# Performance work log

Measured on AMD Instinct MI355X. Metric: run time of the kernel, lower is better.

## Reference

```python
import jax, jax.numpy as jnp
import numpy as np

N_NODES = 50000
N_EDGES = 800000
D = 64
N_LAYERS = 3  # zip(convs(4), batchnorms(3)) truncates to 3 executed layers
N_GRAPHS = 32
EPS_BN = 1e-5
NEG_SLOPE = 0.2


def segment_softmax(logits, seg, n):
    m = jax.ops.segment_max(logits, seg, num_segments=n)
    m = jnp.where(jnp.isfinite(m), m, 0.0)
    z = jnp.exp(logits - m[seg])
    s = jax.ops.segment_sum(z, seg, num_segments=n)
    return z / (s[seg] + 1e-16)


def setup_inputs() -> dict:
    key = jax.random.key(0)
    ks = jax.random.split(key, 16)
    s = 0.1
    return {
        "x": jax.random.normal(ks[0], (N_NODES, D), jnp.float32),
        "edge_index": jax.random.randint(ks[1], (2, N_EDGES), 0, N_NODES),
        "edge_attr": jax.random.normal(ks[2], (N_EDGES, D), jnp.float32),
        "batch": jnp.sort(jax.random.randint(ks[3], (N_NODES,), 0, N_GRAPHS)),
        # EdgeConvLayer MLP params (stacked over layers)
        "em_w1": jax.random.normal(ks[4], (N_LAYERS, 3 * D, D)) * s,
        "em_b1": jnp.zeros((N_LAYERS, D)),
        "em_w2": jax.random.normal(ks[5], (N_LAYERS, D, D)) * s,
        "em_b2": jnp.zeros((N_LAYERS, D)),
        # GATConv params (heads=1, add_self_loops=False)
        "gat_w": jax.random.normal(ks[6], (N_LAYERS, D, D)) * s,
        "att_src": jax.random.normal(ks[7], (N_LAYERS, D)) * s,
        "att_dst": jax.random.normal(ks[8], (N_LAYERS, D)) * s,
        "edge_w": jax.random.normal(ks[9], (N_LAYERS, D, D)) * s,
        "att_edge": jax.random.normal(ks[10], (N_LAYERS, D)) * s,
        "gat_bias": jnp.zeros((N_LAYERS, D)),
        # BatchNorm params
        "bn_gamma": jnp.ones((N_LAYERS, D)),
        "bn_beta": jnp.zeros((N_LAYERS, D)),
        # readout MLP
        "mlp_w1": jax.random.normal(ks[11], (D, D)) * s,
        "mlp_b1": jnp.zeros((D,)),
        "mlp_w2": jax.random.normal(ks[12], (D, D // 2)) * s,
        "mlp_b2": jnp.zeros((D // 2,)),
        "mlp_w3": jax.random.normal(ks[13], (D // 2, 1)) * s,
        "mlp_b3": jnp.zeros((1,)),
    }


def reference(x, edge_index, edge_attr, batch, em_w1, em_b1, em_w2, em_b2,
              gat_w, att_src, att_dst, edge_w, att_edge, gat_bias,
              bn_gamma, bn_beta, mlp_w1, mlp_b1, mlp_w2, mlp_b2, mlp_w3, mlp_b3):
    row, col = edge_index[0], edge_index[1]
    n = x.shape[0]
    for l in range(N_LAYERS):
        # MetaLayer edge model: cat(src, dst, edge_attr) -> 2-layer MLP
        cat = jnp.concatenate([x[row], x[col], edge_attr], axis=1)  # (E, 3D)
        eh = jax.nn.relu(cat @ em_w1[l] + em_b1[l])
        edge_attr = eh @ em_w2[l] + em_b2[l]  # (E, D)
        # GATConv, heads=1: shared linear for src/dst
        xw = x @ gat_w[l]  # (N, D)
        a_edge = edge_attr @ (edge_w[l] @ att_edge[l])  # fused lin_edge + att_edge dot
        logits = (xw @ att_src[l])[row] + (xw @ att_dst[l])[col] + a_edge
        alpha = segment_softmax(jax.nn.leaky_relu(logits, NEG_SLOPE), col, n)
        h = jax.ops.segment_sum(alpha[:, None] * xw[row], col, num_segments=n) + gat_bias[l]
        # BatchNorm (training batch stats) + ReLU
        mu = h.mean(axis=0)
        var = h.var(axis=0)
        x = jax.nn.relu((h - mu) * jax.lax.rsqrt(var + EPS_BN) * bn_gamma[l] + bn_beta[l])
    # global mean pool over graphs
    sums = jax.ops.segment_sum(x, batch, num_segments=N_GRAPHS)
    cnt = jax.ops.segment_sum(jnp.ones((n,), x.dtype), batch, num_segments=N_GRAPHS)
    g = sums / jnp.maximum(cnt, 1.0)[:, None]
    h = jax.nn.relu(g @ mlp_w1 + mlp_b1)
    h = jax.nn.relu(h @ mlp_w2 + mlp_b2)
    return h @ mlp_w3 + mlp_b3  # (N_GRAPHS, 1)
```

## Files before the change

### kernel.cpp

```cpp
#include <hip/hip_runtime.h>


#define NN 50000
#define NE 800000
#define DP 68
#define NEG_SLOPE 0.2f

typedef __attribute__((ext_vector_type(8))) __bf16 bf16x8;
typedef __attribute__((ext_vector_type(4))) float f32x4;

__device__ __forceinline__ float4 ld4(const float* __restrict__ p){ return *(const float4* __restrict__)p; }
__device__ __forceinline__ void st4(float* __restrict__ p, float4 v){ *(float4* __restrict__)p = v; }
__device__ __forceinline__ float4 f4zero(){ return make_float4(0.f,0.f,0.f,0.f); }
__device__ __forceinline__ float4 f4add(float4 a, float4 b){
  return make_float4(a.x+b.x, a.y+b.y, a.z+b.z, a.w+b.w);
}
__device__ __forceinline__ float4 f4fma(float a, float4 b, float4 c){
  return make_float4(fmaf(a,b.x,c.x), fmaf(a,b.y,c.y), fmaf(a,b.z,c.z), fmaf(a,b.w,c.w));
}
__device__ __forceinline__ float f4dot(float4 a, float4 b){
  return fmaf(a.x,b.x, fmaf(a.y,b.y, fmaf(a.z,b.z, a.w*b.w)));
}
__device__ __forceinline__ bf16x8 cvt8(float4 a, float4 b){
  bf16x8 r;
  r[0]=(__bf16)a.x; r[1]=(__bf16)a.y; r[2]=(__bf16)a.z; r[3]=(__bf16)a.w;
  r[4]=(__bf16)b.x; r[5]=(__bf16)b.y; r[6]=(__bf16)b.z; r[7]=(__bf16)b.w;
  return r;
}
__device__ __forceinline__ bf16x8 addpack8(bf16x8 a, bf16x8 b){
  bf16x8 r;
#pragma unroll
  for (int e = 0; e < 8; ++e) r[e] = (__bf16)((float)a[e] + (float)b[e]);
  return r;
}
__device__ __forceinline__ ushort4 pack4(float4 v){
  ushort4 u;
  u.x = __builtin_bit_cast(unsigned short, (__bf16)v.x);
  u.y = __builtin_bit_cast(unsigned short, (__bf16)v.y);
  u.z = __builtin_bit_cast(unsigned short, (__bf16)v.z);
  u.w = __builtin_bit_cast(unsigned short, (__bf16)v.w);
  return u;
}
__device__ __forceinline__ float4 bnrelu4(float4 v, const float* sc, const float* sh, int d){
  return make_float4(
    fmaxf(fmaf(v.x, sc[d+0], sh[d+0]), 0.f),
    fmaxf(fmaf(v.y, sc[d+1], sh[d+1]), 0.f),
    fmaxf(fmaf(v.z, sc[d+2], sh[d+2]), 0.f),
    fmaxf(fmaf(v.w, sc[d+3], sh[d+3]), 0.f));
}

__device__ __forceinline__ void gemm_tile(const float* inT, const float* W,
                                          int el0, int d0, float4 acc[4]){
#pragma unroll 4
  for (int kc = 0; kc < 16; ++kc){
    float4 w0 = ld4(&W[(kc*4+0)*64 + d0]);
    float4 w1 = ld4(&W[(kc*4+1)*64 + d0]);
    float4 w2 = ld4(&W[(kc*4+2)*64 + d0]);
    float4 w3 = ld4(&W[(kc*4+3)*64 + d0]);
#pragma unroll
    for (int i = 0; i < 4; ++i){
      float4 iv = ld4(&inT[(el0+i)*DP + kc*4]);
      acc[i] = f4fma(iv.x, w0, acc[i]);
      acc[i] = f4fma(iv.y, w1, acc[i]);
      acc[i] = f4fma(iv.z, w2, acc[i]);
      acc[i] = f4fma(iv.w, w3, acc[i]);
    }
  }
}

__global__ __launch_bounds__(256) void hist_kernel(const int* __restrict__ ei_col,
                                                   int* __restrict__ cnt){
  int e = blockIdx.x * 256 + threadIdx.x;
  atomicAdd(&cnt[ei_col[e]], 1);
}

__global__ __launch_bounds__(256) void scan_kernel(const int* __restrict__ cnt,
                                                   int* __restrict__ off){
  __shared__ int wsum[4];
  __shared__ int carry_s;
  const int t = threadIdx.x;
  const int lane = t & 63, w = t >> 6;
  if (t == 0) carry_s = 0;
  __syncthreads();
  for (int base = 0; base < NN; base += 256){
    int idx = base + t;
    int v = (idx < NN) ? cnt[idx] : 0;
    int x = v;
#pragma unroll
    for (int o = 1; o < 64; o <<= 1){
      int u = __shfl_up(x, o);
      if (lane >= o) x += u;
    }
    if (lane == 63) wsum[w] = x;
    __syncthreads();
    int wo = carry_s;
#pragma unroll
    for (int k = 0; k < 4; ++k) if (k < w) wo += wsum[k];
    int incl = x + wo;
    if (idx < NN) off[idx] = incl - v;
    __syncthreads();
    if (t == 255) carry_s = incl;
    __syncthreads();
  }
  if (t == 0) off[NN] = carry_s;
}

__global__ __launch_bounds__(256) void scatter_kernel(
    const int* __restrict__ ei, const int* __restrict__ off, int* __restrict__ cur,
    int* __restrict__ srow, int* __restrict__ scol, int* __restrict__ perm){
  int e = blockIdx.x * 256 + threadIdx.x;
  int r = ei[e], c = ei[NE + e];
  int pos = off[c] + atomicAdd(&cur[c], 1);
  srow[pos] = r; scol[pos] = c; perm[pos] = e;
}

__global__ __launch_bounds__(256) void graph_bounds(const int* __restrict__ batch,
                                                    int* __restrict__ goff){
  int n = blockIdx.x * 256 + threadIdx.x;
  if (n >= NN) return;
  int bn = batch[n];
  int bp = (n == 0) ? -1 : batch[n-1];
  for (int g = bp + 1; g <= bn; ++g) goff[g] = n;
  if (n == NN - 1){ for (int g = bn + 1; g <= 32; ++g) goff[g] = NN; }
}

__global__ __launch_bounds__(256) void prep_weights(
    const float* __restrict__ em_w1, const float* __restrict__ em_w2,
    const float* __restrict__ edge_w, const float* __restrict__ att_edge,
    __bf16* __restrict__ w1f, __bf16* __restrict__ w2f, float* __restrict__ vbuf)
{
  const int l = blockIdx.x, t = threadIdx.x;
  const float* W1 = em_w1 + l*12288 + 8192;
  const float* W2 = em_w2 + l*4096;
  for (int p = t; p < 512; p += 256){
    int li = p & 63, ks = (p >> 6) & 1, nt = p >> 7;
    int kbase = ks*32 + (li >> 4)*8;
    int j = nt*16 + (li & 15);
    bf16x8 v1, v2;
#pragma unroll
    for (int e = 0; e < 8; ++e){
      v1[e] = (__bf16)W1[(size_t)(kbase+e)*64 + j];
      v2[e] = (__bf16)W2[(size_t)(kbase+e)*64 + j];
    }
    *(bf16x8*)(w1f + (size_t)l*4096 + p*8) = v1;
    *(bf16x8*)(w2f + (size_t)l*4096 + p*8) = v2;
  }
  if (t < 64){
    float a = 0.f;
    const float* ew = edge_w + l*4096 + t*64;
    const float* ae = att_edge + l*64;
#pragma unroll 8
    for (int j = 0; j < 64; ++j) a = fmaf(ew[j], ae[j], a);
    vbuf[l*64 + t] = a;
  }
}

__global__ __launch_bounds__(256) void node_prep(
    const float* __restrict__ x0_in, const float* __restrict__ h_in,
    const float* __restrict__ musum, const float* __restrict__ sqsum,
    const float* __restrict__ gamma, const float* __restrict__ beta,
    const float* __restrict__ em_w1, const float* __restrict__ em_b1,
    const float* __restrict__ gat_w,
    const float* __restrict__ att_src, const float* __restrict__ att_dst,
    __bf16* __restrict__ xaH, __bf16* __restrict__ xbH, __bf16* __restrict__ xwH,
    float* __restrict__ ssrc, float* __restrict__ sdst, int l)
{
  __shared__ float xt[64*DP];
  __shared__ float Ws[64*64];
  __shared__ float asrc[64], adst[64], b1s[64];
  __shared__ float sc[64], sh[64];
  const int t = threadIdx.x;
  const int n0 = blockIdx.x * 64;
  const int p = blockIdx.y;

  if (l > 0){
    if (t < 64){
      float mu  = musum[t] * (1.0f / NN);
      float var = sqsum[t] * (1.0f / NN) - mu * mu;
      float iv  = rsqrtf(var + 1e-5f) * gamma[(l-1)*64 + t];
      sc[t] = iv;
      sh[t] = beta[(l-1)*64 + t] - mu * iv;
    }
    __syncthreads();
  }

  { int nl = t >> 2, q = t & 3;
    int n = n0 + nl;
    float4 v0, v1, v2, v3;
    if (n < NN){
      const float* src = ((l == 0) ? x0_in : h_in) + (size_t)n*64 + q*16;
      v0 = ld4(src); v1 = ld4(src+4); v2 = ld4(src+8); v3 = ld4(src+12);
      if (l > 0){
        v0 = bnrelu4(v0, sc, sh, q*16);
        v1 = bnrelu4(v1, sc, sh, q*16+4);
        v2 = bnrelu4(v2, sc, sh, q*16+8);
        v3 = bnrelu4(v3, sc, sh, q*16+12);
      }
    } else { v0 = v1 = v2 = v3 = f4zero(); }
    float* dst = &xt[nl*DP + q*16];
    st4(dst, v0); st4(dst+4, v1); st4(dst+8, v2); st4(dst+12, v3);
  }
  if (p == 2){
    if (t < 64) asrc[t] = att_src[l*64 + t];
    else if (t < 128) adst[t-64] = att_dst[l*64 + (t-64)];
  } else if (p == 0 && t < 64){
    b1s[t] = em_b1[l*64 + t];
  }
  const float* wp = (p == 0) ? (em_w1 + l*12288)
                  : (p == 1) ? (em_w1 + l*12288 + 4096)
                             : (gat_w + l*4096);
  for (int i = t; i < 1024; i += 256) st4(&Ws[i*4], ld4(wp + i*4));
  __syncthreads();

  const int nl0 = (t >> 4) << 2;
  const int d0  = (t & 15) << 2;
  __bf16* op = (p == 0) ? xaH : (p == 1) ? xbH : xwH;

  float4 acc[4] = {f4zero(), f4zero(), f4zero(), f4zero()};
  gemm_tile(xt, Ws, nl0, d0, acc);
  if (p == 0){
    float4 bb = ld4(&b1s[d0]);
#pragma unroll
    for (int i = 0; i < 4; ++i) acc[i] = f4add(acc[i], bb);
  }
#pragma unroll
  for (int i = 0; i < 4; ++i){
    int n = n0 + nl0 + i;
    if (n < NN) *(ushort4*)(op + (size_t)n*64 + d0) = pack4(acc[i]);
  }
  if (p == 2){
    float4 a4 = ld4(&asrc[d0]);
    float4 b4 = ld4(&adst[d0]);
    float ps[4], pd[4];
#pragma unroll
    for (int i = 0; i < 4; ++i){ ps[i] = f4dot(acc[i], a4); pd[i] = f4dot(acc[i], b4); }
#pragma unroll
    for (int off = 8; off; off >>= 1){
#pragma unroll
      for (int i = 0; i < 4; ++i){ ps[i] += __shfl_xor(ps[i], off); pd[i] += __shfl_xor(pd[i], off); }
    }
    if ((t & 15) == 0){
#pragma unroll
      for (int i = 0; i < 4; ++i){
        int n = n0 + nl0 + i;
        if (n < NN){ ssrc[n] = ps[i]; sdst[n] = pd[i]; }
      }
    }
  }
}

__global__ __launch_bounds__(256) void edge_mlp(
    const float* __restrict__ ea0,
    const __bf16* ea_in,
    __bf16* ea_out,
    const __bf16* __restrict__ xaH, const __bf16* __restrict__ xbH,
    const float* __restrict__ ssrc, const float* __restrict__ sdst,
    const int* __restrict__ srow, const int* __restrict__ scol,
    const int* __restrict__ permp,
    const __bf16* __restrict__ w1f, const __bf16* __restrict__ w2f,
    const float* __restrict__ b2v, const float* __restrict__ vv,
    float* __restrict__ lrelu, int store_ea)
{
  __shared__ __align__(16) __bf16 uvh[64*72];
  __shared__ __align__(16) unsigned ehw[2048];
  __shared__ float b2s[64], vs[64], sb[128];
  __shared__ int rs[128], cs[128], ps[128];
  const int t = threadIdx.x;
  const int w = t >> 6, l = t & 63, m = l & 15, kg = l >> 4;
  const int eb = blockIdx.x * 128;

  if (t < 128){ rs[t] = srow[eb+t]; cs[t] = scol[eb+t]; }
  else if (t < 192){ b2s[t-128] = b2v[t-128]; vs[t-128] = vv[t-128]; }
  if (permp && t < 128) ps[t] = permp[eb+t];
  __syncthreads();

  const bf16x8* B1 = (const bf16x8*)w1f;
  const bf16x8* B2 = (const bf16x8*)w2f;
  const f32x4 z4 = {0.f, 0.f, 0.f, 0.f};
  const int e_loc = t >> 2, q = t & 3;

  const int r0 = rs[e_loc],      c0 = cs[e_loc];
  const int r1 = rs[64 + e_loc], c1 = cs[64 + e_loc];
  const bf16x8* pa0 = (const bf16x8*)(xaH + (size_t)r0*64 + q*16);
  const bf16x8* pb0 = (const bf16x8*)(xbH + (size_t)c0*64 + q*16);
  const bf16x8* pa1 = (const bf16x8*)(xaH + (size_t)r1*64 + q*16);
  const bf16x8* pb1 = (const bf16x8*)(xbH + (size_t)c1*64 + q*16);
  bf16x8 g_a0l = pa0[0], g_a0h = pa0[1], g_b0l = pb0[0], g_b0h = pb0[1];
  bf16x8 g_a1l = pa1[0], g_a1h = pa1[1], g_b1l = pb1[0], g_b1h = pb1[1];
  float sb0 = 0.f, sb1 = 0.f;
  if (q == 0){ sb0 = ssrc[r0] + sdst[c0]; sb1 = ssrc[r1] + sdst[c1]; }

  bf16x8 A00, A01, A10, A11;
  { const int elA = 16*w + m;
    if (ea0){
      const float* s0 = ea0 + (size_t)ps[elA]*64 + kg*8;
      const float* s1 = ea0 + (size_t)ps[64+elA]*64 + kg*8;
      A00 = cvt8(ld4(s0),    ld4(s0+4));  A01 = cvt8(ld4(s0+32), ld4(s0+36));
      A10 = cvt8(ld4(s1),    ld4(s1+4));  A11 = cvt8(ld4(s1+32), ld4(s1+36));
    } else {
      const __bf16* s0 = ea_in + (size_t)(eb+elA)*64 + kg*8;
      const __bf16* s1 = ea_in + (size_t)(eb+64+elA)*64 + kg*8;
      A00 = *(const bf16x8*)s0;  A01 = *(const bf16x8*)(s0+32);
      A10 = *(const bf16x8*)s1;  A11 = *(const bf16x8*)(s1+32);
    }
  }

  *(bf16x8*)&uvh[e_loc*72 + q*16]     = addpack8(g_a0l, g_b0l);
  *(bf16x8*)&uvh[e_loc*72 + q*16 + 8] = addpack8(g_a0h, g_b0h);
  if (q == 0){ sb[e_loc] = sb0; sb[64 + e_loc] = sb1; }
  asm volatile("" ::: "memory");

  __bf16* esc = (__bf16*)ehw;
  auto tile_compute = [&](bf16x8 a0, bf16x8 a1, int tb){
    f32x4 acc[4];
#pragma unroll
    for (int nt = 0; nt < 4; ++nt){
      acc[nt] = __builtin_amdgcn_mfma_f32_16x16x32_bf16(a0, B1[(nt*2+0)*64 + l], z4, 0, 0, 0);
      acc[nt] = __builtin_amdgcn_mfma_f32_16x16x32_bf16(a1, B1[(nt*2+1)*64 + l], acc[nt], 0, 0, 0);
    }
#pragma unroll
    for (int nt = 0; nt < 4; ++nt){
      const int j = nt*16 + m;
#pragma unroll
      for (int r = 0; r < 4; ++r){
        const int erow = 16*w + 4*kg + r;
        float v = acc[nt][r] + (float)uvh[erow*72 + j];
        v = fmaxf(v, 0.f);
        const int piece = (w*2 + (nt>>1))*64 + (((nt&1)<<1) | (m>>3))*16 + 4*kg + r;
        esc[piece*8 + (m&7)] = (__bf16)v;
      }
    }
    asm volatile("" ::: "memory");
    bf16x8 a20 = *(const bf16x8*)(esc + (size_t)((w*2+0)*64 + kg*16 + m)*8);
    bf16x8 a21 = *(const bf16x8*)(esc + (size_t)((w*2+1)*64 + kg*16 + m)*8);
    f32x4 acc2[4];
#pragma unroll
    for (int nt = 0; nt < 4; ++nt){
      acc2[nt] = __builtin_amdgcn_mfma_f32_16x16x32_bf16(a20, B2[(nt*2+0)*64 + l], z4, 0, 0, 0);
      acc2[nt] = __builtin_amdgcn_mfma_f32_16x16x32_bf16(a21, B2[(nt*2+1)*64 + l], acc2[nt], 0, 0, 0);
    }
    float p0 = 0.f, p1 = 0.f, p2 = 0.f, p3 = 0.f;
#pragma unroll
    for (int nt = 0; nt < 4; ++nt){
      const int j = nt*16 + m;
      const float bj = b2s[j], vj = vs[j];
      float vr[4];
      vr[0] = acc2[nt][0] + bj; vr[1] = acc2[nt][1] + bj;
      vr[2] = acc2[nt][2] + bj; vr[3] = acc2[nt][3] + bj;
      if (store_ea){
        const size_t rowb = (size_t)(eb + tb + 16*w + 4*kg)*64 + (j & ~1);
#pragma unroll
        for (int r = 0; r < 4; ++r){
          unsigned short hu = __builtin_bit_cast(unsigned short, (__bf16)vr[r]);
          int pu = __shfl_xor((int)hu, 1);
          if (!(m & 1)){
            unsigned word = (unsigned)hu | ((unsigned)(pu & 0xffff) << 16);
            *(unsigned*)(ea_out + rowb + (size_t)r*64) = word;
          }
        }
      }
      p0 = fmaf(vr[0], vj, p0); p1 = fmaf(vr[1], vj, p1);
      p2 = fmaf(vr[2], vj, p2); p3 = fmaf(vr[3], vj, p3);
    }
#pragma unroll
    for (int o = 8; o; o >>= 1){
      p0 += __shfl_xor(p0, o); p1 += __shfl_xor(p1, o);
      p2 += __shfl_xor(p2, o); p3 += __shfl_xor(p3, o);
    }
    if (m == 0){
      float pv[4] = {p0, p1, p2, p3};
#pragma unroll
      for (int r = 0; r < 4; ++r){
        const int erow = 16*w + 4*kg + r;
        float logit = sb[tb + erow] + pv[r];
        lrelu[eb + tb + erow] = logit > 0.f ? logit : NEG_SLOPE * logit;
      }
    }
  };

  tile_compute(A00, A01, 0);
  asm volatile("" ::: "memory");
  *(bf16x8*)&uvh[e_loc*72 + q*16]     = addpack8(g_a1l, g_b1l);
  *(bf16x8*)&uvh[e_loc*72 + q*16 + 8] = addpack8(g_a1h, g_b1h);
  asm volatile("" ::: "memory");
  tile_compute(A10, A11, 64);
}

__global__ __launch_bounds__(256) void col_agg(
    const float* __restrict__ lrelu, const int* __restrict__ srow,
    const int* __restrict__ off, const __bf16* __restrict__ xwH,
    float* __restrict__ h)
{
  __shared__ float zS[4][128];
  __shared__ int   rS[4][128];
  const int t = threadIdx.x;
  const int lane = t & 63;
  const int wv = t >> 6;
  const int c = blockIdx.x * 4 + wv;
  const int s0 = off[c], s1 = off[c+1];
  const int L = s1 - s0;

  float l0 = (lane < L)    ? lrelu[s0+lane]    : -3.402823466e38f;
  float l1 = (lane+64 < L) ? lrelu[s0+64+lane] : -3.402823466e38f;
  int   r0 = (lane < L)    ? srow[s0+lane]     : 0;
  int   r1 = (lane+64 < L) ? srow[s0+64+lane]  : 0;

  float m = fmaxf(l0, l1);
  for (int i = lane+128; i < L; i += 64) m = fmaxf(m, lrelu[s0+i]);
#pragma unroll
  for (int o = 32; o; o >>= 1) m = fmaxf(m, __shfl_xor(m, o));

  float z0 = (lane < L)    ? expf(l0 - m) : 0.f;
  float z1 = (lane+64 < L) ? expf(l1 - m) : 0.f;
  float s = z0 + z1;
  for (int i = lane+128; i < L; i += 64) s += expf(lrelu[s0+i] - m);
#pragma unroll
  for (int o = 32; o; o >>= 1) s += __shfl_xor(s, o);
  const float inv = 1.f / (s + 1e-16f);

  zS[wv][lane] = z0;  zS[wv][64+lane] = z1;
  rS[wv][lane] = r0;  rS[wv][64+lane] = r1;
  asm volatile("" ::: "memory");

  float hv0 = 0.f, hv1 = 0.f, hv2 = 0.f, hv3 = 0.f;
  float hv4 = 0.f, hv5 = 0.f, hv6 = 0.f, hv7 = 0.f;
  if (L <= 128){
    int i = 0;
    for (; i + 8 <= L; i += 8){
      float za = zS[wv][i],   zb = zS[wv][i+1], zc = zS[wv][i+2], zd = zS[wv][i+3];
      float ze = zS[wv][i+4], zf = zS[wv][i+5], zg = zS[wv][i+6], zh = zS[wv][i+7];
      int   ra = rS[wv][i],   rb = rS[wv][i+1], rc = rS[wv][i+2], rd = rS[wv][i+3];
      int   re = rS[wv][i+4], rf = rS[wv][i+5], rg = rS[wv][i+6], rh = rS[wv][i+7];
      hv0 = fmaf(za, (float)xwH[(size_t)ra*64 + lane], hv0);
      hv1 = fmaf(zb, (float)xwH[(size_t)rb*64 + lane], hv1);
      hv2 = fmaf(zc, (float)xwH[(size_t)rc*64 + lane], hv2);
      hv3 = fmaf(zd, (float)xwH[(size_t)rd*64 + lane], hv3);
      hv4 = fmaf(ze, (float)xwH[(size_t)re*64 + lane], hv4);
      hv5 = fmaf(zf, (float)xwH[(size_t)rf*64 + lane], hv5);
      hv6 = fmaf(zg, (float)xwH[(size_t)rg*64 + lane], hv6);
      hv7 = fmaf(zh, (float)xwH[(size_t)rh*64 + lane], hv7);
    }
    for (; i < L; ++i)
      hv0 = fmaf(zS[wv][i], (float)xwH[(size_t)rS[wv][i]*64 + lane], hv0);
  } else {
    for (int i = 0; i < L; ++i){
      float z = expf(lrelu[s0+i] - m);
      int r = srow[s0+i];
      hv0 = fmaf(z, (float)xwH[(size_t)r*64 + lane], hv0);
    }
  }
  float hv = ((hv0 + hv1) + (hv2 + hv3)) + ((hv4 + hv5) + (hv6 + hv7));
  h[(size_t)c*64 + lane] = hv * inv;
}

__global__ __launch_bounds__(256) void bn_stats(
    const float* __restrict__ h, float* __restrict__ musum, float* __restrict__ sqsum)
{
  const int t = threadIdx.x;
  const int d = t & 63, sub = t >> 6;
  const int base = blockIdx.x * 256;
  float s = 0.f, s2 = 0.f;
  for (int i = sub; i < 256; i += 4){
    int n = base + i;
    if (n < NN){ float v = h[(size_t)n*64 + d]; s += v; s2 = fmaf(v, v, s2); }
  }
  __shared__ float r1[4][64], r2[4][64];
  r1[sub][d] = s; r2[sub][d] = s2;
  __syncthreads();
  if (sub == 0){
    s  = r1[0][d] + r1[1][d] + r1[2][d] + r1[3][d];
    s2 = r2[0][d] + r2[1][d] + r2[2][d] + r2[3][d];
    atomicAdd(&musum[d], s);
    atomicAdd(&sqsum[d], s2);
  }
}

__global__ __launch_bounds__(256) void seg_pool(
    const float* __restrict__ h, const int* __restrict__ goff,
    const float* __restrict__ musum, const float* __restrict__ sqsum,
    const float* __restrict__ gamma2, const float* __restrict__ beta2,
    float* __restrict__ pools, float* __restrict__ pcnt)
{
  const int g = blockIdx.x;
  const int t = threadIdx.x;
  const int d = t & 63, sub = t >> 6;
  const int s0 = goff[g], s1 = goff[g+1];
  float mu  = musum[d] * (1.0f / NN);
  float var = sqsum[d] * (1.0f / NN) - mu * mu;
  float iv  = rsqrtf(var + 1e-5f) * gamma2[d];
  float shv = beta2[d] - mu * iv;
  float s = 0.f;
  for (int n = s0 + sub; n < s1; n += 4)
    s += fmaxf(fmaf(h[(size_t)n*64 + d], iv, shv), 0.f);
  __shared__ float r[4][64];
  r[sub][d] = s;
  __syncthreads();
  if (sub == 0){
    s = r[0][d] + r[1][d] + r[2][d] + r[3][d];
    pools[g*64 + d] = s;
    if (d == 0) pcnt[g] = (float)(s1 - s0);
  }
}

__global__ __launch_bounds__(256) void final_mlp(
    const float* __restrict__ pools, const float* __restrict__ pcnt,
    const float* __restrict__ w1, const float* __restrict__ b1,
    const float* __restrict__ w2, const float* __restrict__ b2,
    const float* __restrict__ w3, const float* __restrict__ b3,
    float* __restrict__ out)
{
  __shared__ float g[32*64], h1[32*64], h2[32*32];
  const int t = threadIdx.x;
  for (int i = t; i < 2048; i += 256) g[i] = pools[i] / fmaxf(pcnt[i >> 6], 1.0f);
  __syncthreads();
  for (int i = t; i < 2048; i += 256){
    int gi = i >> 6, d = i & 63;
    float a = b1[d];
    for (int k = 0; k < 64; ++k) a = fmaf(g[gi*64 + k], w1[k*64 + d], a);
    h1[i] = fmaxf(a, 0.f);
  }
  __syncthreads();
  for (int i = t; i < 1024; i += 256){
    int gi = i >> 5, d = i & 31;
    float a = b2[d];
    for (int k = 0; k < 64; ++k) a = fmaf(h1[gi*64 + k], w2[k*32 + d], a);
    h2[i] = fmaxf(a, 0.f);
  }
  __syncthreads();
  if (t < 32){
    float a = b3[0];
    for (int k = 0; k < 32; ++k) a = fmaf(h2[t*32 + k], w3[k], a);
    out[t] = a;
  }
}

extern "C" void kernel_launch(void* const* d_in, const int* in_sizes, int n_in,
                              void* d_out, int out_size, void* d_ws, size_t ws_size,
                              hipStream_t stream)
{
  (void)in_sizes; (void)n_in; (void)out_size; (void)ws_size;
  const float* x0       = (const float*)d_in[0];
  const int*   ei       = (const int*)  d_in[1];
  const float* ea0      = (const float*)d_in[2];
  const int*   batch    = (const int*)  d_in[3];
  const float* em_w1    = (const float*)d_in[4];
  const float* em_b1    = (const float*)d_in[5];
  const float* em_w2    = (const float*)d_in[6];
  const float* em_b2    = (const float*)d_in[7];
  const float* gat_w    = (const float*)d_in[8];
  const float* att_src  = (const float*)d_in[9];
  const float* att_dst  = (const float*)d_in[10];
  const float* edge_w   = (const float*)d_in[11];
  const float* att_edge = (const float*)d_in[12];
  const float* bn_gamma = (const float*)d_in[14];
  const float* bn_beta  = (const float*)d_in[15];
  const float* mlp_w1   = (const float*)d_in[16];
  const float* mlp_b1   = (const float*)d_in[17];
  const float* mlp_w2   = (const float*)d_in[18];
  const float* mlp_b2   = (const float*)d_in[19];
  const float* mlp_w3   = (const float*)d_in[20];
  const float* mlp_b3   = (const float*)d_in[21];
  float* out = (float*)d_out;

  const size_t N64 = (size_t)NN * 64, E64 = (size_t)NE * 64;
  float* ws    = (float*)d_ws;
  float* wsE   = ws;
  float* sxa   = wsE + E64;
  float* sxb   = sxa + N64;
  float* sxw   = sxb + N64;
  float* hbuf  = sxw + N64;
  float* musum = hbuf + N64;
  float* sqsum = musum + 64;
  float* lrelu = sqsum + 64;
  float* pools = lrelu + NE;
  float* pcnt  = pools + 2048;
  float* ssrc  = pcnt + 32;
  float* sdst  = ssrc + NN;
  int*   cnt   = (int*)(sdst + NN);
  int*   cur   = cnt + NN;
  int*   soff  = cur + NN;
  int*   srow  = soff + NN + 1;
  int*   scol  = srow + NE;
  int*   perm  = scol + NE;
  int*   goff  = perm + NE;
  __bf16* eaB  = (__bf16*)wsE;
  __bf16* xaH  = (__bf16*)sxa;
  __bf16* xbH  = (__bf16*)sxb;
  __bf16* xwH  = (__bf16*)sxw;
  __bf16* w1f  = (__bf16*)(goff + 40);
  __bf16* w2f  = w1f + 3*4096;
  float* vbuf  = (float*)(w2f + 3*4096);

  hipMemsetAsync(cnt, 0, 2 * NN * sizeof(int), stream);
  hist_kernel<<<NE / 256, 256, 0, stream>>>(ei + NE, cnt);
  scan_kernel<<<1, 256, 0, stream>>>(cnt, soff);
  scatter_kernel<<<NE / 256, 256, 0, stream>>>(ei, soff, cur, srow, scol, perm);
  graph_bounds<<<(NN + 255) / 256, 256, 0, stream>>>(batch, goff);
  prep_weights<<<3, 256, 0, stream>>>(em_w1, em_w2, edge_w, att_edge, w1f, w2f, vbuf);

  for (int l = 0; l < 3; ++l){
    dim3 npg((NN + 63) / 64, 3);
    node_prep<<<npg, 256, 0, stream>>>(
        x0, hbuf, musum, sqsum, bn_gamma, bn_beta,
        em_w1, em_b1, gat_w, att_src, att_dst, xaH, xbH, xwH, ssrc, sdst, l);

    hipMemsetAsync(musum, 0, 128 * sizeof(float), stream);

    edge_mlp<<<NE / 128, 256, 0, stream>>>(
        (l == 0) ? ea0 : nullptr, eaB, eaB, xaH, xbH, ssrc, sdst,
        srow, scol, (l == 0) ? perm : nullptr,
        w1f + (size_t)l*4096, w2f + (size_t)l*4096,
        em_b2 + l*64, vbuf + l*64, lrelu, (l < 2) ? 1 : 0);

    col_agg<<<NN / 4, 256, 0, stream>>>(lrelu, srow, soff, xwH, hbuf);

    bn_stats<<<(NN + 255) / 256, 256, 0, stream>>>(hbuf, musum, sqsum);
  }

  seg_pool<<<32, 256, 0, stream>>>(hbuf, goff, musum, sqsum,
                                   bn_gamma + 128, bn_beta + 128, pools, pcnt);
  final_mlp<<<1, 256, 0, stream>>>(pools, pcnt, mlp_w1, mlp_b1, mlp_w2, mlp_b2,
                                   mlp_w3, mlp_b3, out);
}
```

Before: 813.5 us.

## Merge setup kernels, drop BN atomics and memsets, widen scan, bound edge_mlp

The histogram, graph-bounds and weight-prep kernels are fused into one setup launch, and the single-block scan now uses 1024 threads. BatchNorm statistics are written as 64 per-block partials that consumers reduce, replacing float atomics and removing the per-layer memset. edge_mlp gets a launch bound requesting 8 blocks per CU, which may force register spills. The goal is fewer launches and less serial setup time, at the cost of bn_stats running on only 64 blocks.

```diff
diff --git a/kernel.cpp b/kernel.cpp
--- a/kernel.cpp
+++ b/kernel.cpp
@@ -68,21 +68,60 @@
   }
 }
 
-__global__ __launch_bounds__(256) void hist_kernel(const int* __restrict__ ei_col,
-                                                   int* __restrict__ cnt){
-  int e = blockIdx.x * 256 + threadIdx.x;
-  atomicAdd(&cnt[ei_col[e]], 1);
-}
-
-__global__ __launch_bounds__(256) void scan_kernel(const int* __restrict__ cnt,
-                                                   int* __restrict__ off){
-  __shared__ int wsum[4];
+__global__ __launch_bounds__(256) void setup_kernel(
+    const int* __restrict__ ei_col, int* __restrict__ cnt,
+    const int* __restrict__ batch, int* __restrict__ goff,
+    const float* __restrict__ em_w1, const float* __restrict__ em_w2,
+    const float* __restrict__ edge_w, const float* __restrict__ att_edge,
+    __bf16* __restrict__ w1f, __bf16* __restrict__ w2f, float* __restrict__ vbuf)
+{
+  const int b = blockIdx.x, t = threadIdx.x;
+  if (b < NE/256){
+    atomicAdd(&cnt[ei_col[b*256 + t]], 1);
+    int n = b*256 + t;
+    if (n < NN){
+      int bn = batch[n];
+      int bp = (n == 0) ? -1 : batch[n-1];
+      for (int g = bp + 1; g <= bn; ++g) goff[g] = n;
+      if (n == NN - 1){ for (int g = bn + 1; g <= 32; ++g) goff[g] = NN; }
+    }
+  } else {
+    const int l = b - NE/256;
+    const float* W1 = em_w1 + l*12288 + 8192;
+    const float* W2 = em_w2 + l*4096;
+    for (int p = t; p < 512; p += 256){
+      int li = p & 63, ks = (p >> 6) & 1, nt = p >> 7;
+      int kbase = ks*32 + (li >> 4)*8;
+      int j = nt*16 + (li & 15);
+      bf16x8 v1, v2;
+#pragma unroll
+      for (int e = 0; e < 8; ++e){
+        v1[e] = (__bf16)W1[(size_t)(kbase+e)*64 + j];
+        v2[e] = (__bf16)W2[(size_t)(kbase+e)*64 + j];
+      }
+      *(bf16x8*)(w1f + (size_t)l*4096 + p*8) = v1;
+      *(bf16x8*)(w2f + (size_t)l*4096 + p*8) = v2;
+    }
+    if (t < 64){
+      float a = 0.f;
+      const float* ew = edge_w + l*4096 + t*64;
+      const float* ae = att_edge + l*64;
+#pragma unroll 8
+      for (int j = 0; j < 64; ++j) a = fmaf(ew[j], ae[j], a);
+      vbuf[l*64 + t] = a;
+    }
+  }
+}
+
+__global__ __launch_bounds__(1024) void scan_kernel(const int* __restrict__ cnt,
+                                                    int* __restrict__ off){
+  __shared__ int wsum[16];
   __shared__ int carry_s;
   const int t = threadIdx.x;
   const int lane = t & 63, w = t >> 6;
   if (t == 0) carry_s = 0;
   __syncthreads();
-  for (int base = 0; base < NN; base += 256){
+  for (int base = 0; base < NN; base += 1024){
     int idx = base + t;
     int v = (idx < NN) ? cnt[idx] : 0;
     int x = v;
@@ -95,11 +134,11 @@
     __syncthreads();
     int wo = carry_s;
 #pragma unroll
-    for (int k = 0; k < 4; ++k) if (k < w) wo += wsum[k];
+    for (int k = 0; k < 16; ++k) if (k < w) wo += wsum[k];
     int incl = x + wo;
     if (idx < NN) off[idx] = incl - v;
     __syncthreads();
-    if (t == 255) carry_s = incl;
+    if (t == 1023) carry_s = incl;
     __syncthreads();
   }
   if (t == 0) off[NN] = carry_s;
@@ -114,50 +153,9 @@
   srow[pos] = r; scol[pos] = c; perm[pos] = e;
 }
 
-__global__ __launch_bounds__(256) void graph_bounds(const int* __restrict__ batch,
-                                                    int* __restrict__ goff){
-  int n = blockIdx.x * 256 + threadIdx.x;
-  if (n >= NN) return;
-  int bn = batch[n];
-  int bp = (n == 0) ? -1 : batch[n-1];
-  for (int g = bp + 1; g <= bn; ++g) goff[g] = n;
-  if (n == NN - 1){ for (int g = bn + 1; g <= 32; ++g) goff[g] = NN; }
-}
-
-__global__ __launch_bounds__(256) void prep_weights(
-    const float* __restrict__ em_w1, const float* __restrict__ em_w2,
-    const float* __restrict__ edge_w, const float* __restrict__ att_edge,
-    __bf16* __restrict__ w1f, __bf16* __restrict__ w2f, float* __restrict__ vbuf)
-{
-  const int l = blockIdx.x, t = threadIdx.x;
-  const float* W1 = em_w1 + l*12288 + 8192;
-  const float* W2 = em_w2 + l*4096;
-  for (int p = t; p < 512; p += 256){
-    int li = p & 63, ks = (p >> 6) & 1, nt = p >> 7;
-    int kbase = ks*32 + (li >> 4)*8;
-    int j = nt*16 + (li & 15);
-    bf16x8 v1, v2;
-#pragma unroll
-    for (int e = 0; e < 8; ++e){
-      v1[e] = (__bf16)W1[(size_t)(kbase+e)*64 + j];
-      v2[e] = (__bf16)W2[(size_t)(kbase+e)*64 + j];
-    }
-    *(bf16x8*)(w1f + (size_t)l*4096 + p*8) = v1;
-    *(bf16x8*)(w2f + (size_t)l*4096 + p*8) = v2;
-  }
-  if (t < 64){
-    float a = 0.f;
-    const float* ew = edge_w + l*4096 + t*64;
-    const float* ae = att_edge + l*64;
-#pragma unroll 8
-    for (int j = 0; j < 64; ++j) a = fmaf(ew[j], ae[j], a);
-    vbuf[l*64 + t] = a;
-  }
-}
-
 __global__ __launch_bounds__(256) void node_prep(
     const float* __restrict__ x0_in, const float* __restrict__ h_in,
-    const float* __restrict__ musum, const float* __restrict__ sqsum,
+    const float* __restrict__ bnpart,
     const float* __restrict__ gamma, const float* __restrict__ beta,
     const float* __restrict__ em_w1, const float* __restrict__ em_b1,
     const float* __restrict__ gat_w,
@@ -175,8 +173,14 @@
 
   if (l > 0){
     if (t < 64){
-      float mu  = musum[t] * (1.0f / NN);
-      float var = sqsum[t] * (1.0f / NN) - mu * mu;
+      float s = 0.f, s2 = 0.f;
+#pragma unroll 8
+      for (int k = 0; k < 64; ++k){
+        s  += bnpart[k*128 + t];
+        s2 += bnpart[k*128 + 64 + t];
+      }
+      float mu  = s * (1.0f / NN);
+      float var = s2 * (1.0f / NN) - mu * mu;
       float iv  = rsqrtf(var + 1e-5f) * gamma[(l-1)*64 + t];
       sc[t] = iv;
       sh[t] = beta[(l-1)*64 + t] - mu * iv;
@@ -249,7 +253,7 @@
   }
 }
 
-__global__ __launch_bounds__(256) void edge_mlp(
+__global__ __launch_bounds__(256, 8) void edge_mlp(
     const float* __restrict__ ea0,
     const __bf16* ea_in,
     __bf16* ea_out,
@@ -454,15 +458,17 @@
 }
 
 __global__ __launch_bounds__(256) void bn_stats(
-    const float* __restrict__ h, float* __restrict__ musum, float* __restrict__ sqsum)
-{
+    const float* __restrict__ h, float* __restrict__ bnpart)
+{
+  const int g = blockIdx.x;
   const int t = threadIdx.x;
   const int d = t & 63, sub = t >> 6;
-  const int base = blockIdx.x * 256;
+  const int n0 = g * 782;
+  const int n1 = (n0 + 782 < NN) ? n0 + 782 : NN;
   float s = 0.f, s2 = 0.f;
-  for (int i = sub; i < 256; i += 4){
-    int n = base + i;
-    if (n < NN){ float v = h[(size_t)n*64 + d]; s += v; s2 = fmaf(v, v, s2); }
+  for (int n = n0 + sub; n < n1; n += 4){
+    float v = h[(size_t)n*64 + d];
+    s += v; s2 = fmaf(v, v, s2);
   }
   __shared__ float r1[4][64], r2[4][64];
   r1[sub][d] = s; r2[sub][d] = s2;
@@ -470,28 +476,39 @@
   if (sub == 0){
     s  = r1[0][d] + r1[1][d] + r1[2][d] + r1[3][d];
     s2 = r2[0][d] + r2[1][d] + r2[2][d] + r2[3][d];
-    atomicAdd(&musum[d], s);
-    atomicAdd(&sqsum[d], s2);
+    bnpart[g*128 + d]      = s;
+    bnpart[g*128 + 64 + d] = s2;
   }
 }
 
 __global__ __launch_bounds__(256) void seg_pool(
     const float* __restrict__ h, const int* __restrict__ goff,
-    const float* __restrict__ musum, const float* __restrict__ sqsum,
+    const float* __restrict__ bnpart,
     const float* __restrict__ gamma2, const float* __restrict__ beta2,
     float* __restrict__ pools, float* __restrict__ pcnt)
 {
+  __shared__ float sc[64], sh[64];
   const int g = blockIdx.x;
   const int t = threadIdx.x;
   const int d = t & 63, sub = t >> 6;
+  if (t < 64){
+    float s = 0.f, s2 = 0.f;
+#pragma unroll 8
+    for (int k = 0; k < 64; ++k){
+      s  += bnpart[k*128 + t];
+      s2 += bnpart[k*128 + 64 + t];
+    }
+    float mu  = s * (1.0f / NN);
+    float var = s2 * (1.0f / NN) - mu * mu;
+    float iv  = rsqrtf(var + 1e-5f) * gamma2[t];
+    sc[t] = iv;
+    sh[t] = beta2[t] - mu * iv;
+  }
+  __syncthreads();
   const int s0 = goff[g], s1 = goff[g+1];
-  float mu  = musum[d] * (1.0f / NN);
-  float var = sqsum[d] * (1.0f / NN) - mu * mu;
-  float iv  = rsqrtf(var + 1e-5f) * gamma2[d];
-  float shv = beta2[d] - mu * iv;
   float s = 0.f;
   for (int n = s0 + sub; n < s1; n += 4)
-    s += fmaxf(fmaf(h[(size_t)n*64 + d], iv, shv), 0.f);
+    s += fmaxf(fmaf(h[(size_t)n*64 + d], sc[d], sh[d]), 0.f);
   __shared__ float r[4][64];
   r[sub][d] = s;
   __syncthreads();
@@ -569,9 +586,8 @@
   float* sxb   = sxa + N64;
   float* sxw   = sxb + N64;
   float* hbuf  = sxw + N64;
-  float* musum = hbuf + N64;
-  float* sqsum = musum + 64;
-  float* lrelu = sqsum + 64;
+  float* bnpart= hbuf + N64;
+  float* lrelu = bnpart + 64*128;
   float* pools = lrelu + NE;
   float* pcnt  = pools + 2048;
   float* ssrc  = pcnt + 32;
@@ -592,19 +608,16 @@
   float* vbuf  = (float*)(w2f + 3*4096);
 
   hipMemsetAsync(cnt, 0, 2 * NN * sizeof(int), stream);
-  hist_kernel<<<NE / 256, 256, 0, stream>>>(ei + NE, cnt);
-  scan_kernel<<<1, 256, 0, stream>>>(cnt, soff);
+  setup_kernel<<<NE/256 + 3, 256, 0, stream>>>(
+      ei + NE, cnt, batch, goff, em_w1, em_w2, edge_w, att_edge, w1f, w2f, vbuf);
+  scan_kernel<<<1, 1024, 0, stream>>>(cnt, soff);
   scatter_kernel<<<NE / 256, 256, 0, stream>>>(ei, soff, cur, srow, scol, perm);
-  graph_bounds<<<(NN + 255) / 256, 256, 0, stream>>>(batch, goff);
-  prep_weights<<<3, 256, 0, stream>>>(em_w1, em_w2, edge_w, att_edge, w1f, w2f, vbuf);
 
   for (int l = 0; l < 3; ++l){
     dim3 npg((NN + 63) / 64, 3);
     node_prep<<<npg, 256, 0, stream>>>(
-        x0, hbuf, musum, sqsum, bn_gamma, bn_beta,
+        x0, hbuf, bnpart, bn_gamma, bn_beta,
         em_w1, em_b1, gat_w, att_src, att_dst, xaH, xbH, xwH, ssrc, sdst, l);
-
-    hipMemsetAsync(musum, 0, 128 * sizeof(float), stream);
 
     edge_mlp<<<NE / 128, 256, 0, stream>>>(
         (l == 0) ? ea0 : nullptr, eaB, eaB, xaH, xbH, ssrc, sdst,
@@ -614,10 +627,10 @@
 
     col_agg<<<NN / 4, 256, 0, stream>>>(lrelu, srow, soff, xwH, hbuf);
 
-    bn_stats<<<(NN + 255) / 256, 256, 0, stream>>>(hbuf, musum, sqsum);
-  }
-
-  seg_pool<<<32, 256, 0, stream>>>(hbuf, goff, musum, sqsum,
+    bn_stats<<<64, 256, 0, stream>>>(hbuf, bnpart);
+  }
+
+  seg_pool<<<32, 256, 0, stream>>>(hbuf, goff, bnpart,
                                    bn_gamma + 128, bn_beta + 128, pools, pcnt);
   final_mlp<<<1, 256, 0, stream>>>(pools, pcnt, mlp_w1, mlp_b1, mlp_w2, mlp_b2,
                                    mlp_w3, mlp_b3, out);
```

New measurement: 927.9 us. 1.14x slower.
